# Kernel optimization log

Measured on AMD Instinct MI355X. Metric: run time of the kernel, lower is better.

Reference implementation:

```python
import jax, jax.numpy as jnp
import numpy as np

N_NODES = 50000
N_EDGES = 600000
IN_F = 128
HID_F = 128
OUT_F = 128


def setup_inputs() -> dict:
    key = jax.random.key(0)
    ks = jax.random.split(key, 12)
    features = jax.random.normal(ks[0], (N_NODES, IN_F), dtype=jnp.float32)
    src = jax.random.randint(ks[1], (N_EDGES,), 0, N_NODES, dtype=jnp.int32)
    dst = jax.random.randint(ks[2], (N_EDGES,), 0, N_NODES, dtype=jnp.int32)

    def lin(k, fan_in, fan_out):
        s = 1.0 / jnp.sqrt(fan_in)
        return jax.random.uniform(k, (fan_in, fan_out), jnp.float32, -s, s)

    return {
        "features": features, "src": src, "dst": dst,
        "W1_self": lin(ks[3], IN_F, HID_F), "W1_neigh": lin(ks[4], IN_F, HID_F),
        "b1": jnp.zeros((HID_F,), jnp.float32),
        "W2_self": lin(ks[5], HID_F, HID_F), "W2_neigh": lin(ks[6], HID_F, HID_F),
        "b2": jnp.zeros((HID_F,), jnp.float32),
        "W3_self": lin(ks[7], HID_F, OUT_F), "W3_neigh": lin(ks[8], HID_F, OUT_F),
        "b3": jnp.zeros((OUT_F,), jnp.float32),
    }


def _sage_mean(x, src, dst, W_self, W_neigh, b):
    # gather source-node features along edges, mean-reduce into dst nodes
    msgs = x[src]                                                # [E, d]
    summed = jax.ops.segment_sum(msgs, dst, num_segments=N_NODES)  # [N, d]
    deg = jax.ops.segment_sum(jnp.ones((dst.shape[0],), x.dtype), dst,
                              num_segments=N_NODES)               # [N]
    mean = summed / jnp.maximum(deg, 1.0)[:, None]
    return x @ W_self + mean @ W_neigh + b


def reference(features, src, dst,
              W1_self, W1_neigh, b1,
              W2_self, W2_neigh, b2,
              W3_self, W3_neigh, b3):
    x = features.reshape(features.shape[0], -1)  # Flatten (no-op for 2D)
    x = jax.nn.relu(_sage_mean(x, src, dst, W1_self, W1_neigh, b1))
    x = jax.nn.relu(_sage_mean(x, src, dst, W2_self, W2_neigh, b2))
    x = _sage_mean(x, src, dst, W3_self, W3_neigh, b3)
    return x
```

## Files before the change

### kernel.cpp

```cpp
#include <hip/hip_runtime.h>

#define NN 50000
#define NE 600000
#define F 128

typedef __attribute__((ext_vector_type(4))) float f4;
typedef __attribute__((ext_vector_type(4))) float f32x4;
typedef __bf16 bf16x8 __attribute__((ext_vector_type(8)));
typedef short short8v __attribute__((ext_vector_type(8)));
typedef unsigned short u16x8 __attribute__((ext_vector_type(8)));

__device__ inline ushort f2bf(float f) {
    uint u = __builtin_bit_cast(uint, f);
    uint r = (u + 0x7FFFu + ((u >> 16) & 1u)) >> 16;
    return (ushort)r;
}
__device__ inline float bf2f(ushort u) {
    uint t = ((uint)u) << 16;
    return __builtin_bit_cast(float, t);
}


__global__ void count_deg(const int* __restrict__ dst, int* __restrict__ deg, int E) {
    int e = blockIdx.x * blockDim.x + threadIdx.x;
    if (e < E) atomicAdd(&deg[dst[e]], 1);
}

__global__ __launch_bounds__(1024) void scan_part1(const int* __restrict__ deg,
                                                   int* __restrict__ bsum, int N) {
    __shared__ int ws[16];
    int tid = threadIdx.x;
    int idx = blockIdx.x * 1024 + tid;
    int v = (idx < N) ? deg[idx] : 0;
    #pragma unroll
    for (int o = 32; o; o >>= 1) v += __shfl_down(v, o);
    if ((tid & 63) == 0) ws[tid >> 6] = v;
    __syncthreads();
    if (tid < 64) {
        int t = (tid < 16) ? ws[tid] : 0;
        #pragma unroll
        for (int o = 8; o; o >>= 1) t += __shfl_down(t, o);
        if (tid == 0) bsum[blockIdx.x] = t;
    }
}

__global__ __launch_bounds__(1024) void scan_part3(const int* __restrict__ deg,
                                                   const int* __restrict__ bsum,
                                                   int* __restrict__ off,
                                                   int* __restrict__ cur,
                                                   float* __restrict__ recip,
                                                   int N, int NB) {
    __shared__ int wsum[16];
    __shared__ int sbase;
    int tid = threadIdx.x;
    int wid = tid >> 6;
    int lane = tid & 63;
    if (tid < 64) {
        int v = (tid < NB) ? bsum[tid] : 0;
        int x = v;
        #pragma unroll
        for (int o = 1; o < 64; o <<= 1) {
            int t = __shfl_up(x, o);
            if (lane >= o) x += t;
        }
        if (tid == blockIdx.x) sbase = x - v;
    }
    int idx = blockIdx.x * 1024 + tid;
    int v = (idx < N) ? deg[idx] : 0;
    int x = v;
    #pragma unroll
    for (int o = 1; o < 64; o <<= 1) {
        int t = __shfl_up(x, o);
        if (lane >= o) x += t;
    }
    if (lane == 63) wsum[wid] = x;
    __syncthreads();
    if (tid == 0) {
        int a = 0;
        #pragma unroll
        for (int w = 0; w < 16; ++w) { int t = wsum[w]; wsum[w] = a; a += t; }
    }
    __syncthreads();
    int incl = x + wsum[wid];
    if (idx < N) {
        int start = sbase + incl - v;
        off[idx] = start;
        cur[idx] = start;
        recip[idx] = 1.0f / (float)max(v, 1);
    }
}

__global__ void fill_csr(const int* __restrict__ src, const int* __restrict__ dst,
                         int* __restrict__ cur, int* __restrict__ csr, int E) {
    int e = blockIdx.x * blockDim.x + threadIdx.x;
    if (e < E) {
        int pos = atomicAdd(&cur[dst[e]], 1);
        csr[pos] = src[e];
    }
}


__global__ __launch_bounds__(256) void wt_prep(const float* __restrict__ W1s, const float* __restrict__ W1n,
                                               const float* __restrict__ W2s, const float* __restrict__ W2n,
                                               const float* __restrict__ W3s, const float* __restrict__ W3n,
                                               ushort* __restrict__ Bt1, ushort* __restrict__ Bt2,
                                               ushort* __restrict__ Bt3) {
    int layer = blockIdx.y;
    const float* Ws = (layer == 0) ? W1s : (layer == 1) ? W2s : W3s;
    const float* Wn = (layer == 0) ? W1n : (layer == 1) ? W2n : W3n;
    ushort* Bt = (layer == 0) ? Bt1 : (layer == 1) ? Bt2 : Bt3;
    int col = blockIdx.x;
    int k = threadIdx.x;
    float v = (k < 128) ? Ws[k * 128 + col] : Wn[(k - 128) * 128 + col];
    Bt[col * 256 + k] = f2bf(v);
}


__global__ __launch_bounds__(256) void to_bf16(const float* __restrict__ in,
                                               ushort* __restrict__ out, int n8) {
    int i = blockIdx.x * 256 + threadIdx.x;
    if (i < n8) {
        const f4* p = (const f4*)in + (size_t)i * 2;
        f4 a = p[0], b = p[1];
        short8v w;
        w[0] = (short)f2bf(a[0]); w[1] = (short)f2bf(a[1]);
        w[2] = (short)f2bf(a[2]); w[3] = (short)f2bf(a[3]);
        w[4] = (short)f2bf(b[0]); w[5] = (short)f2bf(b[1]);
        w[6] = (short)f2bf(b[2]); w[7] = (short)f2bf(b[3]);
        ((short8v*)out)[i] = w;
    }
}


template <int RELU, int OUTBF>
__global__ __launch_bounds__(256) void sage_layer(const ushort* __restrict__ xb,
                                                  const int* __restrict__ off,
                                                  const int* __restrict__ deg,
                                                  const float* __restrict__ recip,
                                                  const int* __restrict__ csr,
                                                  const ushort* __restrict__ Bt,
                                                  const float* __restrict__ bias,
                                                  void* __restrict__ outp, int N) {
    __shared__ ushort sa[32 * 256];
    int tid = threadIdx.x;
    int r0 = blockIdx.x * 32;

    {
        int row = tid >> 3;
        int c = tid & 7;
        int grow = r0 + row;
        uint sw = ((uint)row & 7u) << 4;
        uint base = (uint)(row * 512 + c * 32);
        short8v w0 = (short8v)0, w1 = (short8v)0;
        if (grow < N) {
            const short8v* sp = (const short8v*)&xb[(size_t)grow * 128 + c * 16];
            w0 = sp[0]; w1 = sp[1];
        }
        *(short8v*)((char*)sa + (base ^ sw)) = w0;
        *(short8v*)((char*)sa + ((base + 16) ^ sw)) = w1;
    }

    {
        int g = tid >> 4;
        int l16 = tid & 15;
        const ushort* xpb = xb + (size_t)l16 * 8;
        #pragma unroll
        for (int rep = 0; rep < 2; ++rep) {
            int row = g + rep * 16;
            int node = r0 + row;
            float a[8] = {0.f, 0.f, 0.f, 0.f, 0.f, 0.f, 0.f, 0.f};
            if (node < N) {
                int start = off[node];
                int d = deg[node];
                int nfull = d & ~7;
                int i = 0;
                for (; i < nfull; i += 8) {
                    int s[8];
                    #pragma unroll
                    for (int u = 0; u < 8; ++u) s[u] = csr[start + i + u];
                    u16x8 v[8];
                    #pragma unroll
                    for (int u = 0; u < 8; ++u) v[u] = *(const u16x8*)(xpb + (size_t)s[u] * 128);
                    #pragma unroll
                    for (int u = 0; u < 8; ++u) {
                        #pragma unroll
                        for (int j = 0; j < 8; ++j) a[j] += bf2f(v[u][j]);
                    }
                }
                if (i < d) {
                    int dm1 = d - 1;
                    int s[8];
                    #pragma unroll
                    for (int u = 0; u < 8; ++u) {
                        int idx = i + u;
                        s[u] = csr[start + ((idx < dm1) ? idx : dm1)];
                    }
                    u16x8 v[8];
                    #pragma unroll
                    for (int u = 0; u < 8; ++u) v[u] = *(const u16x8*)(xpb + (size_t)s[u] * 128);
                    #pragma unroll
                    for (int u = 0; u < 8; ++u) {
                        float m = (i + u < d) ? 1.f : 0.f;
                        #pragma unroll
                        for (int j = 0; j < 8; ++j) a[j] += m * bf2f(v[u][j]);
                    }
                }
                float r = recip[node];
                #pragma unroll
                for (int j = 0; j < 8; ++j) a[j] *= r;
            }
            short8v w;
            #pragma unroll
            for (int j = 0; j < 8; ++j) w[j] = (short)f2bf(a[j]);
            uint sw = ((uint)row & 7u) << 4;
            uint addr = (uint)(row * 512 + 256 + l16 * 16);
            *(short8v*)((char*)sa + (addr ^ sw)) = w;
        }
    }
    __syncthreads();

    int lane = tid & 63;
    int wid = tid >> 6;
    int wr = wid & 1;
    int wc = wid >> 1;
    int l15 = lane & 15;
    int lg = lane >> 4;

    int arow = wr * 16 + l15;
    uint abase = (uint)(arow * 512 + lg * 16);
    uint asw = ((uint)arow & 7u) << 4;
    bf16x8 a[8];
    #pragma unroll
    for (int ks = 0; ks < 8; ++ks) {
        a[ks] = *(const bf16x8*)((const char*)sa + ((abase + (uint)ks * 64) ^ asw));
    }

    f32x4 acc[4];
    #pragma unroll
    for (int ct = 0; ct < 4; ++ct) acc[ct] = (f32x4)0.f;

    #pragma unroll
    for (int ct = 0; ct < 4; ++ct) {
        int bcol = wc * 64 + ct * 16 + l15;
        const ushort* bp = Bt + bcol * 256 + lg * 8;
        #pragma unroll
        for (int ks = 0; ks < 8; ++ks) {
            bf16x8 b = *(const bf16x8*)(bp + ks * 32);
            acc[ct] = __builtin_amdgcn_mfma_f32_16x16x32_bf16(a[ks], b, acc[ct], 0, 0, 0);
        }
    }

    int crow = r0 + wr * 16 + lg * 4;
    #pragma unroll
    for (int ct = 0; ct < 4; ++ct) {
        int col = wc * 64 + ct * 16 + l15;
        float bv = bias[col];
        #pragma unroll
        for (int r = 0; r < 4; ++r) {
            int row = crow + r;
            if (row < N) {
                float v = acc[ct][r] + bv;
                if (RELU) v = fmaxf(v, 0.f);
                if (OUTBF) ((ushort*)outp)[(size_t)row * 128 + col] = f2bf(v);
                else       ((float*)outp)[(size_t)row * 128 + col] = v;
            }
        }
    }
}


extern "C" void kernel_launch(void* const* d_in, const int* in_sizes, int n_in,
                              void* d_out, int out_size, void* d_ws, size_t ws_size,
                              hipStream_t stream) {
    const float* feat = (const float*)d_in[0];
    const int* src = (const int*)d_in[1];
    const int* dst = (const int*)d_in[2];
    const float* W1s = (const float*)d_in[3];
    const float* W1n = (const float*)d_in[4];
    const float* b1 = (const float*)d_in[5];
    const float* W2s = (const float*)d_in[6];
    const float* W2n = (const float*)d_in[7];
    const float* b2 = (const float*)d_in[8];
    const float* W3s = (const float*)d_in[9];
    const float* W3n = (const float*)d_in[10];
    const float* b3 = (const float*)d_in[11];
    float* out = (float*)d_out;

    const int N = NN, E = NE;
    const int NB = (N + 1023) / 1024;

    char* p = (char*)d_ws;
    auto alloc = [&](size_t bytes) {
        char* q = p;
        p += (bytes + 255) & ~(size_t)255;
        return q;
    };
    int* deg = (int*)alloc((size_t)N * 4);
    int* off = (int*)alloc((size_t)N * 4);
    int* cur = (int*)alloc((size_t)N * 4);
    float* recip = (float*)alloc((size_t)N * 4);
    int* bsum = (int*)alloc(64 * 4);
    int* csr = (int*)alloc((size_t)E * 4);
    ushort* xb0 = (ushort*)alloc((size_t)N * F * 2);
    ushort* h1b = (ushort*)alloc((size_t)N * F * 2);
    ushort* h2b = (ushort*)alloc((size_t)N * F * 2);
    ushort* Bt1 = (ushort*)alloc(128 * 256 * 2);
    ushort* Bt2 = (ushort*)alloc(128 * 256 * 2);
    ushort* Bt3 = (ushort*)alloc(128 * 256 * 2);

    wt_prep<<<dim3(128, 3), 256, 0, stream>>>(W1s, W1n, W2s, W2n, W3s, W3n, Bt1, Bt2, Bt3);
    to_bf16<<<(N * F / 8 + 255) / 256, 256, 0, stream>>>(feat, xb0, N * F / 8);

    hipMemsetAsync(deg, 0, (size_t)N * 4, stream);
    count_deg<<<(E + 255) / 256, 256, 0, stream>>>(dst, deg, E);
    scan_part1<<<NB, 1024, 0, stream>>>(deg, bsum, N);
    scan_part3<<<NB, 1024, 0, stream>>>(deg, bsum, off, cur, recip, N, NB);
    fill_csr<<<(E + 255) / 256, 256, 0, stream>>>(src, dst, cur, csr, E);

    int grid = (N + 31) / 32;

    sage_layer<1, 1><<<grid, 256, 0, stream>>>(xb0, off, deg, recip, csr, Bt1, b1, h1b, N);
    sage_layer<1, 1><<<grid, 256, 0, stream>>>(h1b, off, deg, recip, csr, Bt2, b2, h2b, N);
    sage_layer<0, 0><<<grid, 256, 0, stream>>>(h2b, off, deg, recip, csr, Bt3, b3, out, N);
}
```

Before: 244.3 us.

## Overlap self-feature MFMA with neighbor gather by splitting the fused SAGE GEMM

```diff
diff --git a/kernel.cpp b/kernel.cpp
--- a/kernel.cpp
+++ b/kernel.cpp
@@ -159,64 +159,6 @@
         *(short8v*)((char*)sa + (base ^ sw)) = w0;
         *(short8v*)((char*)sa + ((base + 16) ^ sw)) = w1;
     }
-
-    {
-        int g = tid >> 4;
-        int l16 = tid & 15;
-        const ushort* xpb = xb + (size_t)l16 * 8;
-        #pragma unroll
-        for (int rep = 0; rep < 2; ++rep) {
-            int row = g + rep * 16;
-            int node = r0 + row;
-            float a[8] = {0.f, 0.f, 0.f, 0.f, 0.f, 0.f, 0.f, 0.f};
-            if (node < N) {
-                int start = off[node];
-                int d = deg[node];
-                int nfull = d & ~7;
-                int i = 0;
-                for (; i < nfull; i += 8) {
-                    int s[8];
-                    #pragma unroll
-                    for (int u = 0; u < 8; ++u) s[u] = csr[start + i + u];
-                    u16x8 v[8];
-                    #pragma unroll
-                    for (int u = 0; u < 8; ++u) v[u] = *(const u16x8*)(xpb + (size_t)s[u] * 128);
-                    #pragma unroll
-                    for (int u = 0; u < 8; ++u) {
-                        #pragma unroll
-                        for (int j = 0; j < 8; ++j) a[j] += bf2f(v[u][j]);
-                    }
-                }
-                if (i < d) {
-                    int dm1 = d - 1;
-                    int s[8];
-                    #pragma unroll
-                    for (int u = 0; u < 8; ++u) {
-                        int idx = i + u;
-                        s[u] = csr[start + ((idx < dm1) ? idx : dm1)];
-                    }
-                    u16x8 v[8];
-                    #pragma unroll
-                    for (int u = 0; u < 8; ++u) v[u] = *(const u16x8*)(xpb + (size_t)s[u] * 128);
-                    #pragma unroll
-                    for (int u = 0; u < 8; ++u) {
-                        float m = (i + u < d) ? 1.f : 0.f;
-                        #pragma unroll
-                        for (int j = 0; j < 8; ++j) a[j] += m * bf2f(v[u][j]);
-                    }
-                }
-                float r = recip[node];
-                #pragma unroll
-                for (int j = 0; j < 8; ++j) a[j] *= r;
-            }
-            short8v w;
-            #pragma unroll
-            for (int j = 0; j < 8; ++j) w[j] = (short)f2bf(a[j]);
-            uint sw = ((uint)row & 7u) << 4;
-            uint addr = (uint)(row * 512 + 256 + l16 * 16);
-            *(short8v*)((char*)sa + (addr ^ sw)) = w;
-        }
-    }
     __syncthreads();
 
     int lane = tid & 63;
@@ -225,28 +167,132 @@
     int wc = wid >> 1;
     int l15 = lane & 15;
     int lg = lane >> 4;
+    int l16 = tid & 15;
+    int g = tid >> 4;
+
+    const ushort* xpb = xb + (size_t)l16 * 8;
+
+    int nodeA = r0 + g;
+    int startA = 0, dA = 0;
+    float rA = 0.f;
+    if (nodeA < N) { startA = off[nodeA]; dA = deg[nodeA]; rA = recip[nodeA]; }
+    int dm1A = (dA > 0) ? dA - 1 : 0;
+    int baseA = (dA > 0) ? startA : 0;
+    u16x8 vA[8];
+    {
+        int s[8];
+        #pragma unroll
+        for (int u = 0; u < 8; ++u) {
+            int idx = (u < dm1A) ? u : dm1A;
+            s[u] = csr[baseA + idx];
+        }
+        #pragma unroll
+        for (int u = 0; u < 8; ++u) vA[u] = *(const u16x8*)(xpb + (size_t)s[u] * 128);
+    }
 
     int arow = wr * 16 + l15;
     uint abase = (uint)(arow * 512 + lg * 16);
     uint asw = ((uint)arow & 7u) << 4;
-    bf16x8 a[8];
-    #pragma unroll
-    for (int ks = 0; ks < 8; ++ks) {
-        a[ks] = *(const bf16x8*)((const char*)sa + ((abase + (uint)ks * 64) ^ asw));
-    }
-
+    bf16x8 ax[4];
+    #pragma unroll
+    for (int ks = 0; ks < 4; ++ks) {
+        ax[ks] = *(const bf16x8*)((const char*)sa + ((abase + (uint)ks * 64) ^ asw));
+    }
     f32x4 acc[4];
     #pragma unroll
     for (int ct = 0; ct < 4; ++ct) acc[ct] = (f32x4)0.f;
-
     #pragma unroll
     for (int ct = 0; ct < 4; ++ct) {
         int bcol = wc * 64 + ct * 16 + l15;
         const ushort* bp = Bt + bcol * 256 + lg * 8;
         #pragma unroll
-        for (int ks = 0; ks < 8; ++ks) {
+        for (int ks = 0; ks < 4; ++ks) {
             bf16x8 b = *(const bf16x8*)(bp + ks * 32);
-            acc[ct] = __builtin_amdgcn_mfma_f32_16x16x32_bf16(a[ks], b, acc[ct], 0, 0, 0);
+            acc[ct] = __builtin_amdgcn_mfma_f32_16x16x32_bf16(ax[ks], b, acc[ct], 0, 0, 0);
+        }
+    }
+
+    {
+        float a[8] = {0.f, 0.f, 0.f, 0.f, 0.f, 0.f, 0.f, 0.f};
+        #pragma unroll
+        for (int u = 0; u < 8; ++u) {
+            float m = (u < dA) ? 1.f : 0.f;
+            #pragma unroll
+            for (int j = 0; j < 8; ++j) a[j] += m * bf2f(vA[u][j]);
+        }
+        for (int i = 8; i < dA; i += 8) {
+            int s[8];
+            #pragma unroll
+            for (int u = 0; u < 8; ++u) {
+                int idx = i + u;
+                s[u] = csr[baseA + ((idx < dm1A) ? idx : dm1A)];
+            }
+            u16x8 v[8];
+            #pragma unroll
+            for (int u = 0; u < 8; ++u) v[u] = *(const u16x8*)(xpb + (size_t)s[u] * 128);
+            #pragma unroll
+            for (int u = 0; u < 8; ++u) {
+                float m = (i + u < dA) ? 1.f : 0.f;
+                #pragma unroll
+                for (int j = 0; j < 8; ++j) a[j] += m * bf2f(v[u][j]);
+            }
+        }
+        short8v w;
+        #pragma unroll
+        for (int j = 0; j < 8; ++j) w[j] = (short)f2bf(a[j] * rA);
+        uint sw = ((uint)g & 7u) << 4;
+        uint addr = (uint)(g * 512 + 256 + l16 * 16);
+        *(short8v*)((char*)sa + (addr ^ sw)) = w;
+    }
+
+    {
+        int rowB = g + 16;
+        int nodeB = r0 + rowB;
+        int startB = 0, dB = 0;
+        float rB = 0.f;
+        if (nodeB < N) { startB = off[nodeB]; dB = deg[nodeB]; rB = recip[nodeB]; }
+        int dm1B = (dB > 0) ? dB - 1 : 0;
+        int baseB = (dB > 0) ? startB : 0;
+        float a[8] = {0.f, 0.f, 0.f, 0.f, 0.f, 0.f, 0.f, 0.f};
+        for (int i = 0; i < dB; i += 8) {
+            int s[8];
+            #pragma unroll
+            for (int u = 0; u < 8; ++u) {
+                int idx = i + u;
+                s[u] = csr[baseB + ((idx < dm1B) ? idx : dm1B)];
+            }
+            u16x8 v[8];
+            #pragma unroll
+            for (int u = 0; u < 8; ++u) v[u] = *(const u16x8*)(xpb + (size_t)s[u] * 128);
+            #pragma unroll
+            for (int u = 0; u < 8; ++u) {
+                float m = (i + u < dB) ? 1.f : 0.f;
+                #pragma unroll
+                for (int j = 0; j < 8; ++j) a[j] += m * bf2f(v[u][j]);
+            }
+        }
+        short8v w;
+        #pragma unroll
+        for (int j = 0; j < 8; ++j) w[j] = (short)f2bf(a[j] * rB);
+        uint sw = ((uint)rowB & 7u) << 4;
+        uint addr = (uint)(rowB * 512 + 256 + l16 * 16);
+        *(short8v*)((char*)sa + (addr ^ sw)) = w;
+    }
+    __syncthreads();
+
+    bf16x8 am[4];
+    #pragma unroll
+    for (int ks = 0; ks < 4; ++ks) {
+        am[ks] = *(const bf16x8*)((const char*)sa + ((abase + 256u + (uint)ks * 64) ^ asw));
+    }
+    #pragma unroll
+    for (int ct = 0; ct < 4; ++ct) {
+        int bcol = wc * 64 + ct * 16 + l15;
+        const ushort* bp = Bt + bcol * 256 + 128 + lg * 8;
+        #pragma unroll
+        for (int ks = 0; ks < 4; ++ks) {
+            bf16x8 b = *(const bf16x8*)(bp + ks * 32);
+            acc[ct] = __builtin_amdgcn_mfma_f32_16x16x32_bf16(am[ks], b, acc[ct], 0, 0, 0);
         }
     }
 
```

New measurement: 234.4 us. 1.04x faster.
